# Optimization experiments

Hardware: AMD Instinct MI355X
Metric: run time of the kernel (lower is better)

## Reference

```python
import jax, jax.numpy as jnp
import numpy as np

L = 4           # num_layers
H = 1536        # hidden_size
NQ = 12         # num_q_heads
NKV = 2         # num_kv_heads
D = 128         # head_dim
I = 8960        # mlp intermediate
S = 2048        # q_len == max_seq_len (full prefill, past_kv_len = 0)
EPS = 1e-6
SCALE = 1.0 / np.sqrt(D)


def setup_inputs() -> dict:
    key = jax.random.key(0)
    ks = jax.random.split(key, 16)
    hidden_states = jax.random.normal(ks[0], (1, S, H), dtype=jnp.float32)
    # real RoPE tables (base 10000), duplicated-half layout like HF Qwen2
    inv_freq = 1.0 / (10000.0 ** (np.arange(0, D, 2, dtype=np.float32) / D))
    t = np.arange(S, dtype=np.float32)
    freqs = np.outer(t, inv_freq)                      # [S, D/2]
    emb = np.concatenate([freqs, freqs], axis=-1)      # [S, D]
    position_cos = jnp.asarray(np.cos(emb))[None]      # [1, S, D]
    position_sin = jnp.asarray(np.sin(emb))[None]
    # causal additive mask [1, 1, S, S]
    causal = jnp.tril(jnp.ones((S, S), dtype=bool))
    attention_mask = jnp.where(causal, 0.0, -1e9).astype(jnp.float32)[None, None]
    sd = 0.02
    Wq = sd * jax.random.normal(ks[1], (L, H, NQ * D), dtype=jnp.float32)
    bq = jnp.zeros((L, NQ * D), dtype=jnp.float32)
    Wk = sd * jax.random.normal(ks[2], (L, H, NKV * D), dtype=jnp.float32)
    bk = jnp.zeros((L, NKV * D), dtype=jnp.float32)
    Wv = sd * jax.random.normal(ks[3], (L, H, NKV * D), dtype=jnp.float32)
    bv = jnp.zeros((L, NKV * D), dtype=jnp.float32)
    Wo = sd * jax.random.normal(ks[4], (L, NQ * D, H), dtype=jnp.float32)
    Wgate = sd * jax.random.normal(ks[5], (L, H, I), dtype=jnp.float32)
    Wup = sd * jax.random.normal(ks[6], (L, H, I), dtype=jnp.float32)
    Wdown = sd * jax.random.normal(ks[7], (L, I, H), dtype=jnp.float32)
    ln1_w = jnp.ones((L, H), dtype=jnp.float32)
    ln2_w = jnp.ones((L, H), dtype=jnp.float32)
    final_ln_w = jnp.ones((H,), dtype=jnp.float32)
    return dict(hidden_states=hidden_states, position_cos=position_cos,
                position_sin=position_sin, attention_mask=attention_mask,
                Wq=Wq, bq=bq, Wk=Wk, bk=bk, Wv=Wv, bv=bv, Wo=Wo,
                Wgate=Wgate, Wup=Wup, Wdown=Wdown,
                ln1_w=ln1_w, ln2_w=ln2_w, final_ln_w=final_ln_w)


def rms_norm(x, w):
    return x * jax.lax.rsqrt(jnp.mean(x * x, axis=-1, keepdims=True) + EPS) * w


def rotate_half(x):
    x1, x2 = jnp.split(x, 2, axis=-1)
    return jnp.concatenate([-x2, x1], axis=-1)


def reference(hidden_states, position_cos, position_sin, attention_mask,
              Wq, bq, Wk, bk, Wv, bv, Wo, Wgate, Wup, Wdown,
              ln1_w, ln2_w, final_ln_w):
    cos = position_cos[:, None]  # [1, 1, S, D]
    sin = position_sin[:, None]
    x = hidden_states
    rep = NQ // NKV
    for i in range(L):
        residual = x
        h = rms_norm(x, ln1_w[i])
        q = (h @ Wq[i] + bq[i]).reshape(1, S, NQ, D).transpose(0, 2, 1, 3)   # [1,NQ,S,D]
        k = (h @ Wk[i] + bk[i]).reshape(1, S, NKV, D).transpose(0, 2, 1, 3)  # [1,NKV,S,D]
        v = (h @ Wv[i] + bv[i]).reshape(1, S, NKV, D).transpose(0, 2, 1, 3)
        q = q * cos + rotate_half(q) * sin
        k = k * cos + rotate_half(k) * sin
        # KV cache write is fp16; full prefill so cache == current k/v (fp16 roundtrip)
        k_full = k.astype(jnp.float16).astype(jnp.float32)
        v_full = v.astype(jnp.float16).astype(jnp.float32)
        k_full = jnp.repeat(k_full, rep, axis=1)  # GQA expand -> [1,NQ,S,D]
        v_full = jnp.repeat(v_full, rep, axis=1)
        scores = jnp.einsum('bhqd,bhkd->bhqk', q, k_full) * SCALE + attention_mask
        probs = jax.nn.softmax(scores, axis=-1)
        attn = jnp.einsum('bhqk,bhkd->bhqd', probs, v_full)
        attn = attn.transpose(0, 2, 1, 3).reshape(1, S, NQ * D)
        x = residual + attn @ Wo[i]
        residual = x
        h = rms_norm(x, ln2_w[i])
        x = residual + (jax.nn.silu(h @ Wgate[i]) * (h @ Wup[i])) @ Wdown[i]
    return rms_norm(x, final_ln_w)
```

## Files before the change

kernel.cpp:

```cpp
#include <hip/hip_runtime.h>

#define S_LEN 2048
#define H_DIM 1536
#define NQ_H 12
#define NKV_H 2
#define HD 128
#define I_DIM 8960
#define QKV_N 2048
#define GU_N 17920
#define SCALE 0.08838834764831845f

typedef _Float16 f16;
typedef _Float16 f16x8 __attribute__((ext_vector_type(8)));
typedef float f32x4 __attribute__((ext_vector_type(4)));

__device__ __forceinline__ void gload16(const void* g, void* l) {
  __builtin_amdgcn_global_load_lds((__attribute__((address_space(1))) void*)g,
                                   (__attribute__((address_space(3))) void*)l,
                                   16, 0, 0);
}

template <int MODE>
__global__ __launch_bounds__(256) void gemm_bt(const f16* __restrict__ A,
                                               const f16* __restrict__ BT,
                                               float* __restrict__ Cf,
                                               f16* __restrict__ Ch,
                                               int N, int Ktot, int Kc) {
  __shared__ __attribute__((aligned(16))) f16 As[128 * 32];
  __shared__ __attribute__((aligned(16))) f16 Bs[128 * 32];
  const int tid = threadIdx.x;
  const int w = tid >> 6, lane = tid & 63;
  const int quad = lane >> 4, cc = lane & 15;
  const int wm = w >> 1, wn = w & 1;
  const int m0 = blockIdx.y * 128, n0 = blockIdx.x * 128;
  const int kbase = blockIdx.z * Kc;

  const int c1 = tid, c2 = tid + 256;
  const f16* Ag1 = A + (size_t)(m0 + (c1 >> 2)) * Ktot + kbase + (c1 & 3) * 8;
  const f16* Ag2 = A + (size_t)(m0 + (c2 >> 2)) * Ktot + kbase + (c2 & 3) * 8;
  const f16* Bg1 = BT + (size_t)(n0 + (c1 >> 2)) * Ktot + kbase + (c1 & 3) * 8;
  const f16* Bg2 = BT + (size_t)(n0 + (c2 >> 2)) * Ktot + kbase + (c2 & 3) * 8;
  f16* Al1 = As + (w * 64) * 8;
  f16* Al2 = As + (256 + w * 64) * 8;
  f16* Bl1 = Bs + (w * 64) * 8;
  f16* Bl2 = Bs + (256 + w * 64) * 8;

  const f32x4 fz = {0.f, 0.f, 0.f, 0.f};
  f32x4 acc[4][4];
#pragma unroll
  for (int i = 0; i < 4; ++i)
#pragma unroll
    for (int j = 0; j < 4; ++j) acc[i][j] = fz;

  for (int k0 = 0; k0 < Kc; k0 += 32) {
    __syncthreads();
    gload16(Ag1 + k0, Al1);
    gload16(Ag2 + k0, Al2);
    gload16(Bg1 + k0, Bl1);
    gload16(Bg2 + k0, Bl2);
    __syncthreads();
    f16x8 af[4], bf[4];
#pragma unroll
    for (int i = 0; i < 4; ++i)
      af[i] = *(const f16x8*)(As + (wm * 64 + i * 16 + cc) * 32 + quad * 8);
#pragma unroll
    for (int j = 0; j < 4; ++j)
      bf[j] = *(const f16x8*)(Bs + (wn * 64 + j * 16 + cc) * 32 + quad * 8);
#pragma unroll
    for (int i = 0; i < 4; ++i)
#pragma unroll
      for (int j = 0; j < 4; ++j)
        acc[i][j] = __builtin_amdgcn_mfma_f32_16x16x32_f16(af[i], bf[j], acc[i][j], 0, 0, 0);
  }

#pragma unroll
  for (int i = 0; i < 4; ++i) {
    const int row = m0 + wm * 64 + i * 16 + quad * 4;
#pragma unroll
    for (int j = 0; j < 4; ++j) {
      const int col = n0 + wn * 64 + j * 16 + cc;
#pragma unroll
      for (int r = 0; r < 4; ++r) {
        const size_t idx = (size_t)(row + r) * N + col;
        if (MODE == 1) unsafeAtomicAdd(&Cf[idx], acc[i][j][r]);
        else Ch[idx] = (f16)acc[i][j][r];
      }
    }
  }
}

__global__ __launch_bounds__(256) void transpose_f2h(const float* __restrict__ src,
                                                     f16* __restrict__ dst,
                                                     int K_, int N_) {
  __shared__ float tile[32][33];
  const int c0 = blockIdx.x * 32, r0 = blockIdx.y * 32;
  const int x = threadIdx.x & 31, y4 = threadIdx.x >> 5;
#pragma unroll
  for (int i = 0; i < 4; ++i) {
    int r = r0 + y4 + i * 8;
    if (r < K_ && c0 + x < N_) tile[y4 + i * 8][x] = src[(size_t)r * N_ + c0 + x];
  }
  __syncthreads();
#pragma unroll
  for (int i = 0; i < 4; ++i) {
    int rr = y4 + i * 8;
    int dr = c0 + rr, dc = r0 + x;
    if (dr < N_ && dc < K_) dst[(size_t)dr * K_ + dc] = (f16)tile[x][rr];
  }
}

template <bool OUT_F32>
__global__ __launch_bounds__(256) void rmsnorm_kernel(const float* __restrict__ x,
                                                      const float* __restrict__ w,
                                                      f16* __restrict__ hh,
                                                      float* __restrict__ hf) {
  const int s = blockIdx.x;
  const float* xr = x + (size_t)s * H_DIM;
  float ss = 0.f;
  for (int i = threadIdx.x; i < H_DIM; i += 256) {
    float v = xr[i];
    ss += v * v;
  }
#pragma unroll
  for (int m = 32; m >= 1; m >>= 1) ss += __shfl_xor(ss, m);
  __shared__ float red[4];
  if ((threadIdx.x & 63) == 0) red[threadIdx.x >> 6] = ss;
  __syncthreads();
  ss = red[0] + red[1] + red[2] + red[3];
  const float rr = rsqrtf(ss * (1.0f / H_DIM) + 1e-6f);
  for (int i = threadIdx.x; i < H_DIM; i += 256) {
    float v = xr[i] * rr * w[i];
    if (OUT_F32) hf[(size_t)s * H_DIM + i] = v;
    else hh[(size_t)s * H_DIM + i] = (f16)v;
  }
}

__global__ __launch_bounds__(256) void rope_kernel(const float* __restrict__ qkv,
                                                   const float* __restrict__ cosb,
                                                   const float* __restrict__ sinb,
                                                   const float* __restrict__ bq,
                                                   const float* __restrict__ bk,
                                                   const float* __restrict__ bv,
                                                   f16* __restrict__ q_r,
                                                   f16* __restrict__ k_r,
                                                   f16* __restrict__ v_r) {
  const int s = blockIdx.x;
  const float* row = qkv + (size_t)s * QKV_N;
#pragma unroll
  for (int ci = 0; ci < 8; ++ci) {
    const int col = ci * 256 + threadIdx.x;
    if (col < 1536) {
      const int hh = col >> 7, d = col & 127;
      const int part = (d < 64) ? d + 64 : d - 64;
      const float v0 = row[col] + bq[col];
      const float v1 = row[(hh << 7) + part] + bq[(hh << 7) + part];
      const float cs = cosb[s * HD + d], sn = sinb[s * HD + d];
      const float rot = (d < 64) ? -v1 : v1;
      q_r[((size_t)hh * S_LEN + s) * HD + d] = (f16)(v0 * cs + rot * sn);
    } else if (col < 1792) {
      const int cc2 = col - 1536;
      const int hh = cc2 >> 7, d = cc2 & 127;
      const int part = (d < 64) ? d + 64 : d - 64;
      const float v0 = row[col] + bk[cc2];
      const float v1 = row[1536 + (hh << 7) + part] + bk[(hh << 7) + part];
      const float cs = cosb[s * HD + d], sn = sinb[s * HD + d];
      const float rot = (d < 64) ? -v1 : v1;
      k_r[((size_t)hh * S_LEN + s) * HD + d] = (f16)(v0 * cs + rot * sn);
    } else {
      const int cc2 = col - 1792;
      const int hh = cc2 >> 7, d = cc2 & 127;
      const float v0 = row[col] + bv[cc2];
      v_r[((size_t)hh * HD + d) * S_LEN + s] = (f16)v0;
    }
  }
}

__global__ __launch_bounds__(256) void attn_kernel(const f16* __restrict__ Q,
                                                   const f16* __restrict__ Kc,
                                                   const f16* __restrict__ Vt,
                                                   f16* __restrict__ Oa) {
  __shared__ __attribute__((aligned(16))) f16 ks[64 * 136];
  __shared__ __attribute__((aligned(16))) f16 vs[128 * 72];
  __shared__ __attribute__((aligned(16))) f16 ps[64 * 72];
  const int h = blockIdx.x, qt = blockIdx.y;
  const int hk = h / (NQ_H / NKV_H);
  const int tid = threadIdx.x, w = tid >> 6, lane = tid & 63;
  const int quad = lane >> 4, cc = lane & 15;

  f16x8 qf[4];
  const f16* Qg = Q + ((size_t)h * S_LEN + qt * 64) * HD;
#pragma unroll
  for (int kk = 0; kk < 4; ++kk)
    qf[kk] = *(const f16x8*)(Qg + (size_t)(w * 16 + cc) * HD + kk * 32 + quad * 8);

  const f32x4 fz = {0.f, 0.f, 0.f, 0.f};
  f32x4 o_acc[8];
  float m_run[4], l_run[4];
#pragma unroll
  for (int j = 0; j < 8; ++j) o_acc[j] = fz;
#pragma unroll
  for (int r = 0; r < 4; ++r) { m_run[r] = -1e30f; l_run[r] = 0.f; }

  const int nkt = qt + 1;
  for (int kt = 0; kt < nkt; ++kt) {
    const int kv0 = kt * 64;
    __syncthreads();
    const f16* Kg = Kc + ((size_t)hk * S_LEN + kv0) * HD;
    for (int t = tid; t < 64 * 16; t += 256) {
      int r = t >> 4, ch = t & 15;
      *(uint4*)(ks + r * 136 + ch * 8) = *(const uint4*)(Kg + (size_t)r * HD + ch * 8);
    }
    const f16* Vg = Vt + (size_t)hk * HD * S_LEN + kv0;
    for (int t = tid; t < 128 * 8; t += 256) {
      int r = t >> 3, ch = t & 7;
      *(uint4*)(vs + r * 72 + ch * 8) = *(const uint4*)(Vg + (size_t)r * S_LEN + ch * 8);
    }
    __syncthreads();

    f32x4 sc[4];
#pragma unroll
    for (int j = 0; j < 4; ++j) sc[j] = fz;
#pragma unroll
    for (int kk = 0; kk < 4; ++kk) {
      f16x8 bfr[4];
#pragma unroll
      for (int j = 0; j < 4; ++j)
        bfr[j] = *(const f16x8*)(ks + (j * 16 + cc) * 136 + kk * 32 + quad * 8);
#pragma unroll
      for (int j = 0; j < 4; ++j)
        sc[j] = __builtin_amdgcn_mfma_f32_16x16x32_f16(qf[kk], bfr[j], sc[j], 0, 0, 0);
    }

    const bool need_mask = (kt == qt);
#pragma unroll
    for (int j = 0; j < 4; ++j)
#pragma unroll
      for (int r = 0; r < 4; ++r) {
        float v = sc[j][r] * SCALE;
        if (need_mask) {
          int rowg = qt * 64 + w * 16 + quad * 4 + r;
          int colg = kv0 + j * 16 + cc;
          if (colg > rowg) v = -1e30f;
        }
        sc[j][r] = v;
      }

#pragma unroll
    for (int r = 0; r < 4; ++r) {
      float mx = sc[0][r];
#pragma unroll
      for (int j = 1; j < 4; ++j) mx = fmaxf(mx, sc[j][r]);
      mx = fmaxf(mx, __shfl_xor(mx, 1));
      mx = fmaxf(mx, __shfl_xor(mx, 2));
      mx = fmaxf(mx, __shfl_xor(mx, 4));
      mx = fmaxf(mx, __shfl_xor(mx, 8));
      const float mnew = fmaxf(m_run[r], mx);
      const float alpha = __expf(m_run[r] - mnew);
      m_run[r] = mnew;
      l_run[r] *= alpha;
#pragma unroll
      for (int jd = 0; jd < 8; ++jd) o_acc[jd][r] *= alpha;
      float rs = 0.f;
      const int prow = w * 16 + quad * 4 + r;
#pragma unroll
      for (int j = 0; j < 4; ++j) {
        float p = __expf(sc[j][r] - mnew);
        rs += p;
        ps[prow * 72 + j * 16 + cc] = (f16)p;
      }
      rs += __shfl_xor(rs, 1);
      rs += __shfl_xor(rs, 2);
      rs += __shfl_xor(rs, 4);
      rs += __shfl_xor(rs, 8);
      l_run[r] += rs;
    }

#pragma unroll
    for (int kk = 0; kk < 2; ++kk) {
      f16x8 pa = *(const f16x8*)(ps + (w * 16 + cc) * 72 + kk * 32 + quad * 8);
#pragma unroll
      for (int j = 0; j < 8; ++j) {
        f16x8 vb = *(const f16x8*)(vs + (j * 16 + cc) * 72 + kk * 32 + quad * 8);
        o_acc[j] = __builtin_amdgcn_mfma_f32_16x16x32_f16(pa, vb, o_acc[j], 0, 0, 0);
      }
    }
  }

#pragma unroll
  for (int j = 0; j < 8; ++j)
#pragma unroll
    for (int r = 0; r < 4; ++r) {
      const int rowg = qt * 64 + w * 16 + quad * 4 + r;
      const int colg = j * 16 + cc;
      Oa[(size_t)rowg * H_DIM + h * HD + colg] = (f16)(o_acc[j][r] / l_run[r]);
    }
}

__global__ __launch_bounds__(256) void silu_mul(const f16* __restrict__ gu,
                                                f16* __restrict__ hm) {
  const int i = blockIdx.x * 256 + threadIdx.x;
  const int s = blockIdx.y;
  const float g = (float)gu[(size_t)s * GU_N + i];
  const float u = (float)gu[(size_t)s * GU_N + I_DIM + i];
  const float sig = 1.f / (1.f + __expf(-g));
  hm[(size_t)s * I_DIM + i] = (f16)(g * sig * u);
}

extern "C" void kernel_launch(void* const* d_in, const int* in_sizes, int n_in,
                              void* d_out, int out_size, void* d_ws, size_t ws_size,
                              hipStream_t stream) {
  const float* hidden = (const float*)d_in[0];
  const float* cosb   = (const float*)d_in[1];
  const float* sinb   = (const float*)d_in[2];
  const float* Wq     = (const float*)d_in[4];
  const float* bq     = (const float*)d_in[5];
  const float* Wk     = (const float*)d_in[6];
  const float* bk     = (const float*)d_in[7];
  const float* Wv     = (const float*)d_in[8];
  const float* bv     = (const float*)d_in[9];
  const float* Wo     = (const float*)d_in[10];
  const float* Wg     = (const float*)d_in[11];
  const float* Wu     = (const float*)d_in[12];
  const float* Wd     = (const float*)d_in[13];
  const float* ln1    = (const float*)d_in[14];
  const float* ln2    = (const float*)d_in[15];
  const float* lnf    = (const float*)d_in[16];

  char* wp = (char*)d_ws;
  auto take = [&](size_t bytes) {
    void* p = (void*)wp;
    wp += (bytes + 255) & ~(size_t)255;
    return p;
  };
  f16* wqkvT  = (f16*)take((size_t)QKV_N * H_DIM * 2);
  f16* woT    = (f16*)take((size_t)H_DIM * H_DIM * 2);
  f16* wguT   = (f16*)take((size_t)GU_N * H_DIM * 2);
  f16* wdT    = (f16*)take((size_t)H_DIM * I_DIM * 2);
  float* x    = (float*)take((size_t)S_LEN * H_DIM * 4);
  f16* hbuf   = (f16*)take((size_t)S_LEN * H_DIM * 2);
  float* qkv  = (float*)take((size_t)S_LEN * QKV_N * 4);
  f16* q_r    = (f16*)take((size_t)NQ_H * S_LEN * HD * 2);
  f16* k_r    = (f16*)take((size_t)NKV_H * S_LEN * HD * 2);
  f16* v_r    = (f16*)take((size_t)NKV_H * HD * S_LEN * 2);
  f16* gu     = (f16*)take((size_t)S_LEN * GU_N * 2);
  f16* hmid   = (f16*)take((size_t)S_LEN * I_DIM * 2);

  hipMemcpyAsync(x, hidden, (size_t)S_LEN * H_DIM * 4, hipMemcpyDeviceToDevice, stream);

  for (int l = 0; l < 4; ++l) {
    transpose_f2h<<<dim3(48, 48), 256, 0, stream>>>(Wq + (size_t)l * H_DIM * 1536, wqkvT, H_DIM, 1536);
    transpose_f2h<<<dim3(8, 48), 256, 0, stream>>>(Wk + (size_t)l * H_DIM * 256, wqkvT + (size_t)1536 * H_DIM, H_DIM, 256);
    transpose_f2h<<<dim3(8, 48), 256, 0, stream>>>(Wv + (size_t)l * H_DIM * 256, wqkvT + (size_t)1792 * H_DIM, H_DIM, 256);
    transpose_f2h<<<dim3(48, 48), 256, 0, stream>>>(Wo + (size_t)l * H_DIM * H_DIM, woT, H_DIM, H_DIM);
    transpose_f2h<<<dim3(280, 48), 256, 0, stream>>>(Wg + (size_t)l * H_DIM * I_DIM, wguT, H_DIM, I_DIM);
    transpose_f2h<<<dim3(280, 48), 256, 0, stream>>>(Wu + (size_t)l * H_DIM * I_DIM, wguT + (size_t)I_DIM * H_DIM, H_DIM, I_DIM);
    transpose_f2h<<<dim3(48, 280), 256, 0, stream>>>(Wd + (size_t)l * I_DIM * H_DIM, wdT, I_DIM, H_DIM);

    rmsnorm_kernel<false><<<S_LEN, 256, 0, stream>>>(x, ln1 + l * H_DIM, hbuf, nullptr);
    hipMemsetAsync(qkv, 0, (size_t)S_LEN * QKV_N * 4, stream);
    gemm_bt<1><<<dim3(QKV_N / 128, S_LEN / 128, 2), 256, 0, stream>>>(hbuf, wqkvT, qkv, nullptr, QKV_N, H_DIM, 768);
    rope_kernel<<<S_LEN, 256, 0, stream>>>(qkv, cosb, sinb, bq + l * 1536, bk + l * 256, bv + l * 256, q_r, k_r, v_r);
    attn_kernel<<<dim3(NQ_H, S_LEN / 64), 256, 0, stream>>>(q_r, k_r, v_r, hbuf);
    gemm_bt<1><<<dim3(H_DIM / 128, S_LEN / 128, 4), 256, 0, stream>>>(hbuf, woT, x, nullptr, H_DIM, H_DIM, 384);
    rmsnorm_kernel<false><<<S_LEN, 256, 0, stream>>>(x, ln2 + l * H_DIM, hbuf, nullptr);
    gemm_bt<2><<<dim3(GU_N / 128, S_LEN / 128, 1), 256, 0, stream>>>(hbuf, wguT, nullptr, gu, GU_N, H_DIM, H_DIM);
    silu_mul<<<dim3(I_DIM / 256, S_LEN), 256, 0, stream>>>(gu, hmid);
    gemm_bt<1><<<dim3(H_DIM / 128, S_LEN / 128, 4), 256, 0, stream>>>(hmid, wdT, x, nullptr, H_DIM, I_DIM, 2240);
  }
  rmsnorm_kernel<true><<<S_LEN, 256, 0, stream>>>(x, lnf, nullptr, (float*)d_out);
}
```

Before: 3.098 ms.

## Add 256x256-tile 8-wave GEMM with 4-stage LDS pipeline for QKV, gate/up, down

Adds a new GEMM kernel that uses 256x256 output tiles with 512 threads, each wave computing a 128x64 subtile. It keeps a four-buffer LDS ring with async global-to-LDS loads issued three steps ahead, interleaved with the MFMA work, and uses XOR-swizzled LDS addressing. The QKV, gate/up and down projections now use it, with new split-K factors. This raises operand reuse and overlaps loads with math, at the cost of high register pressure and fewer blocks for the smaller GEMMs.

```diff
diff --git a/kernel.cpp b/kernel.cpp
--- a/kernel.cpp
+++ b/kernel.cpp
@@ -18,6 +18,129 @@
   __builtin_amdgcn_global_load_lds((__attribute__((address_space(1))) void*)g,
                                    (__attribute__((address_space(3))) void*)l,
                                    16, 0, 0);
+}
+
+template <int MODE>
+__global__ __launch_bounds__(512, 2) void gemm256(const f16* __restrict__ A,
+                                                  const f16* __restrict__ BT,
+                                                  float* __restrict__ Cf,
+                                                  f16* __restrict__ Ch,
+                                                  int N, int Ktot, int Kc) {
+  constexpr int TE = 256 * 32;
+  __shared__ __attribute__((aligned(16))) f16 As[4 * TE];
+  __shared__ __attribute__((aligned(16))) f16 Bs[4 * TE];
+  const int tid = threadIdx.x;
+  const int w = tid >> 6, lane = tid & 63;
+  const int quad = lane >> 4, cc = lane & 15;
+  const int wm = w >> 2, wn = w & 3;
+  const int m0 = blockIdx.y * 256, n0 = blockIdx.x * 256;
+  const int kbase = blockIdx.z * Kc;
+  const int NT = Kc >> 5;
+
+  const int lr = lane >> 2, lc = lane & 3;
+  const int cg = lc ^ (lr & 3) ^ ((lr >> 2) & 1);
+  const f16* AgR0 = A + (size_t)(m0 + w * 16 + lr) * Ktot + kbase + cg * 8;
+  const f16* AgR1 = AgR0 + (size_t)128 * Ktot;
+  const f16* BgR0 = BT + (size_t)(n0 + w * 16 + lr) * Ktot + kbase + cg * 8;
+  const f16* BgR1 = BgR0 + (size_t)128 * Ktot;
+  const int ldsl0 = (w * 16) * 32;
+  const int ldsl1 = (128 + w * 16) * 32;
+
+  const int sc8 = (quad ^ (cc & 3) ^ ((cc >> 2) & 1)) * 8;
+
+  const f32x4 fz = {0.f, 0.f, 0.f, 0.f};
+  f32x4 acc[8][4];
+#pragma unroll
+  for (int i = 0; i < 8; ++i)
+#pragma unroll
+    for (int j = 0; j < 4; ++j) acc[i][j] = fz;
+
+#pragma unroll
+  for (int pt = 0; pt < 3; ++pt) {
+    const int kk = pt * 32;
+    gload16(AgR0 + kk, As + pt * TE + ldsl0);
+    gload16(AgR1 + kk, As + pt * TE + ldsl1);
+    gload16(BgR0 + kk, Bs + pt * TE + ldsl0);
+    gload16(BgR1 + kk, Bs + pt * TE + ldsl1);
+  }
+
+  for (int t = 0; t < NT; ++t) {
+    const f16* Ab = As + (t & 3) * TE;
+    const f16* Bb = Bs + (t & 3) * TE;
+    const int ahead = NT - 1 - t;
+    if (ahead >= 2)      asm volatile("s_waitcnt vmcnt(8)" ::: "memory");
+    else if (ahead == 1) asm volatile("s_waitcnt vmcnt(4)" ::: "memory");
+    else                 asm volatile("s_waitcnt vmcnt(0)" ::: "memory");
+    asm volatile("s_barrier" ::: "memory");
+
+    const bool pf = (t + 3) < NT;
+    const int kq = (t + 3) * 32;
+    f16* Apf = As + ((t + 3) & 3) * TE;
+    f16* Bpf = Bs + ((t + 3) & 3) * TE;
+
+    f16x8 bf[4], af0, af1;
+
+    if (pf) gload16(AgR0 + kq, Apf + ldsl0);
+#pragma unroll
+    for (int fc = 0; fc < 4; ++fc)
+      bf[fc] = *(const f16x8*)(Bb + (wn * 64 + fc * 16 + cc) * 32 + sc8);
+    af0 = *(const f16x8*)(Ab + (wm * 128 + 0 * 16 + cc) * 32 + sc8);
+    af1 = *(const f16x8*)(Ab + (wm * 128 + 1 * 16 + cc) * 32 + sc8);
+#pragma unroll
+    for (int fc = 0; fc < 4; ++fc)
+      acc[0][fc] = __builtin_amdgcn_mfma_f32_16x16x32_f16(af0, bf[fc], acc[0][fc], 0, 0, 0);
+#pragma unroll
+    for (int fc = 0; fc < 4; ++fc)
+      acc[1][fc] = __builtin_amdgcn_mfma_f32_16x16x32_f16(af1, bf[fc], acc[1][fc], 0, 0, 0);
+    asm volatile("s_barrier" ::: "memory");
+
+    if (pf) gload16(AgR1 + kq, Apf + ldsl1);
+    af0 = *(const f16x8*)(Ab + (wm * 128 + 2 * 16 + cc) * 32 + sc8);
+    af1 = *(const f16x8*)(Ab + (wm * 128 + 3 * 16 + cc) * 32 + sc8);
+#pragma unroll
+    for (int fc = 0; fc < 4; ++fc)
+      acc[2][fc] = __builtin_amdgcn_mfma_f32_16x16x32_f16(af0, bf[fc], acc[2][fc], 0, 0, 0);
+#pragma unroll
+    for (int fc = 0; fc < 4; ++fc)
+      acc[3][fc] = __builtin_amdgcn_mfma_f32_16x16x32_f16(af1, bf[fc], acc[3][fc], 0, 0, 0);
+    asm volatile("s_barrier" ::: "memory");
+
+    if (pf) gload16(BgR0 + kq, Bpf + ldsl0);
+    af0 = *(const f16x8*)(Ab + (wm * 128 + 4 * 16 + cc) * 32 + sc8);
+    af1 = *(const f16x8*)(Ab + (wm * 128 + 5 * 16 + cc) * 32 + sc8);
+#pragma unroll
+    for (int fc = 0; fc < 4; ++fc)
+      acc[4][fc] = __builtin_amdgcn_mfma_f32_16x16x32_f16(af0, bf[fc], acc[4][fc], 0, 0, 0);
+#pragma unroll
+    for (int fc = 0; fc < 4; ++fc)
+      acc[5][fc] = __builtin_amdgcn_mfma_f32_16x16x32_f16(af1, bf[fc], acc[5][fc], 0, 0, 0);
+    asm volatile("s_barrier" ::: "memory");
+
+    if (pf) gload16(BgR1 + kq, Bpf + ldsl1);
+    af0 = *(const f16x8*)(Ab + (wm * 128 + 6 * 16 + cc) * 32 + sc8);
+    af1 = *(const f16x8*)(Ab + (wm * 128 + 7 * 16 + cc) * 32 + sc8);
+#pragma unroll
+    for (int fc = 0; fc < 4; ++fc)
+      acc[6][fc] = __builtin_amdgcn_mfma_f32_16x16x32_f16(af0, bf[fc], acc[6][fc], 0, 0, 0);
+#pragma unroll
+    for (int fc = 0; fc < 4; ++fc)
+      acc[7][fc] = __builtin_amdgcn_mfma_f32_16x16x32_f16(af1, bf[fc], acc[7][fc], 0, 0, 0);
+  }
+
+#pragma unroll
+  for (int fr = 0; fr < 8; ++fr) {
+    const int row = m0 + wm * 128 + fr * 16 + quad * 4;
+#pragma unroll
+    for (int fc = 0; fc < 4; ++fc) {
+      const int col = n0 + wn * 64 + fc * 16 + cc;
+#pragma unroll
+      for (int r = 0; r < 4; ++r) {
+        const size_t idx = (size_t)(row + r) * N + col;
+        if (MODE == 1) unsafeAtomicAdd(&Cf[idx], acc[fr][fc][r]);
+        else Ch[idx] = (f16)acc[fr][fc][r];
+      }
+    }
+  }
 }
 
 template <int MODE>
@@ -358,14 +481,14 @@
 
     rmsnorm_kernel<false><<<S_LEN, 256, 0, stream>>>(x, ln1 + l * H_DIM, hbuf, nullptr);
     hipMemsetAsync(qkv, 0, (size_t)S_LEN * QKV_N * 4, stream);
-    gemm_bt<1><<<dim3(QKV_N / 128, S_LEN / 128, 2), 256, 0, stream>>>(hbuf, wqkvT, qkv, nullptr, QKV_N, H_DIM, 768);
+    gemm256<1><<<dim3(QKV_N / 256, S_LEN / 256, 4), 512, 0, stream>>>(hbuf, wqkvT, qkv, nullptr, QKV_N, H_DIM, 384);
     rope_kernel<<<S_LEN, 256, 0, stream>>>(qkv, cosb, sinb, bq + l * 1536, bk + l * 256, bv + l * 256, q_r, k_r, v_r);
     attn_kernel<<<dim3(NQ_H, S_LEN / 64), 256, 0, stream>>>(q_r, k_r, v_r, hbuf);
     gemm_bt<1><<<dim3(H_DIM / 128, S_LEN / 128, 4), 256, 0, stream>>>(hbuf, woT, x, nullptr, H_DIM, H_DIM, 384);
     rmsnorm_kernel<false><<<S_LEN, 256, 0, stream>>>(x, ln2 + l * H_DIM, hbuf, nullptr);
-    gemm_bt<2><<<dim3(GU_N / 128, S_LEN / 128, 1), 256, 0, stream>>>(hbuf, wguT, nullptr, gu, GU_N, H_DIM, H_DIM);
+    gemm256<2><<<dim3(GU_N / 256, S_LEN / 256, 1), 512, 0, stream>>>(hbuf, wguT, nullptr, gu, GU_N, H_DIM, H_DIM);
     silu_mul<<<dim3(I_DIM / 256, S_LEN), 256, 0, stream>>>(gu, hmid);
-    gemm_bt<1><<<dim3(H_DIM / 128, S_LEN / 128, 4), 256, 0, stream>>>(hmid, wdT, x, nullptr, H_DIM, I_DIM, 2240);
+    gemm256<1><<<dim3(H_DIM / 256, S_LEN / 256, 5), 512, 0, stream>>>(hmid, wdT, x, nullptr, H_DIM, I_DIM, 1792);
   }
   rmsnorm_kernel<true><<<S_LEN, 256, 0, stream>>>(x, lnf, nullptr, (float*)d_out);
 }
```

After: 3.630 ms. 1.17x slower.

## Add 256x256-tile 4-stage pipelined GEMM for QKV, gate/up and down projections

Applied to the files above, without the earlier changes.

Introduces a 512-thread GEMM kernel with 256x256 output tiles, a 4-slot LDS ring filled by direct global-to-LDS loads three tiles ahead, XOR-swizzled LDS addressing, and raised wave priority around the MFMA block. It is used for the QKV, gate/up and down projections, with split-K factors changed to keep the grid filled. The aim is more operand reuse per LDS load and better hiding of load latency than the 128x128 kernel. In exchange it uses 128 KB of LDS and 128 accumulator registers per thread, which limits occupancy, and the larger tiles give fewer blocks (the gate/up grid is 70x8).

```diff
diff --git a/kernel.cpp b/kernel.cpp
--- a/kernel.cpp
+++ b/kernel.cpp
@@ -18,6 +18,100 @@
   __builtin_amdgcn_global_load_lds((__attribute__((address_space(1))) void*)g,
                                    (__attribute__((address_space(3))) void*)l,
                                    16, 0, 0);
+}
+
+template <int MODE>
+__global__ __launch_bounds__(512, 2) void gemm256(const f16* __restrict__ A,
+                                                  const f16* __restrict__ BT,
+                                                  float* __restrict__ Cf,
+                                                  f16* __restrict__ Ch,
+                                                  int N, int Ktot, int Kc) {
+  constexpr int TS = 256 * 32;
+  __shared__ __attribute__((aligned(16))) f16 As[4 * TS];
+  __shared__ __attribute__((aligned(16))) f16 Bs[4 * TS];
+  const int tid = threadIdx.x;
+  const int w = tid >> 6, lane = tid & 63;
+  const int quad = lane >> 4, cc = lane & 15;
+  const int wm = w >> 2, wn = w & 3;
+  const int m0 = blockIdx.y * 256, n0 = blockIdx.x * 256;
+  const int kbase = blockIdx.z * Kc;
+  const int NT = Kc >> 5;
+
+  const int srow = lane >> 2;
+  const int schk = lane & 3;
+  const int gchk = schk ^ (srow & 3);
+  const f16* Ag = A + (size_t)(m0 + w * 32 + srow) * Ktot + kbase + gchk * 8;
+  const f16* Bg = BT + (size_t)(n0 + w * 32 + srow) * Ktot + kbase + gchk * 8;
+  const int lb = (w * 32) * 32;
+
+  const int rs8 = (quad ^ (cc & 3)) * 8;
+
+  const f32x4 fz = {0.f, 0.f, 0.f, 0.f};
+  f32x4 acc[8][4];
+#pragma unroll
+  for (int i = 0; i < 8; ++i)
+#pragma unroll
+    for (int j = 0; j < 4; ++j) acc[i][j] = fz;
+
+#define STAGE256(slot, tt)                                   \
+  {                                                          \
+    f16* Ad = As + (slot)*TS + lb;                           \
+    f16* Bd = Bs + (slot)*TS + lb;                           \
+    const int ko = (tt)*32;                                  \
+    gload16(Ag + ko, Ad);                                    \
+    gload16(Ag + ko + 16 * Ktot, Ad + 16 * 32);              \
+    gload16(Bg + ko, Bd);                                    \
+    gload16(Bg + ko + 16 * Ktot, Bd + 16 * 32);              \
+  }
+
+  STAGE256(0, 0);
+  STAGE256(1, 1);
+  STAGE256(2, 2);
+
+  for (int t = 0; t < NT; ++t) {
+    const int ahead = NT - 1 - t;
+    if (ahead >= 2)      asm volatile("s_waitcnt vmcnt(8)" ::: "memory");
+    else if (ahead == 1) asm volatile("s_waitcnt vmcnt(4)" ::: "memory");
+    else                 asm volatile("s_waitcnt vmcnt(0)" ::: "memory");
+    asm volatile("s_barrier" ::: "memory");
+
+    const f16* Ab = As + (t & 3) * TS;
+    const f16* Bb = Bs + (t & 3) * TS;
+
+    f16x8 bf[4], af[8];
+#pragma unroll
+    for (int nf = 0; nf < 4; ++nf)
+      bf[nf] = *(const f16x8*)(Bb + (wn * 64 + nf * 16 + cc) * 32 + rs8);
+#pragma unroll
+    for (int mf = 0; mf < 8; ++mf)
+      af[mf] = *(const f16x8*)(Ab + (wm * 128 + mf * 16 + cc) * 32 + rs8);
+
+    __builtin_amdgcn_s_setprio(1);
+#pragma unroll
+    for (int mf = 0; mf < 8; ++mf)
+#pragma unroll
+      for (int nf = 0; nf < 4; ++nf)
+        acc[mf][nf] = __builtin_amdgcn_mfma_f32_16x16x32_f16(af[mf], bf[nf], acc[mf][nf], 0, 0, 0);
+    __builtin_amdgcn_s_setprio(0);
+
+    if (t + 3 < NT) STAGE256((t + 3) & 3, t + 3);
+  }
+#undef STAGE256
+
+#pragma unroll
+  for (int fr = 0; fr < 8; ++fr) {
+    const int row = m0 + wm * 128 + fr * 16 + quad * 4;
+#pragma unroll
+    for (int fc = 0; fc < 4; ++fc) {
+      const int col = n0 + wn * 64 + fc * 16 + cc;
+#pragma unroll
+      for (int r = 0; r < 4; ++r) {
+        const size_t idx = (size_t)(row + r) * N + col;
+        if (MODE == 1) unsafeAtomicAdd(&Cf[idx], acc[fr][fc][r]);
+        else Ch[idx] = (f16)acc[fr][fc][r];
+      }
+    }
+  }
 }
 
 template <int MODE>
@@ -358,14 +452,14 @@
 
     rmsnorm_kernel<false><<<S_LEN, 256, 0, stream>>>(x, ln1 + l * H_DIM, hbuf, nullptr);
     hipMemsetAsync(qkv, 0, (size_t)S_LEN * QKV_N * 4, stream);
-    gemm_bt<1><<<dim3(QKV_N / 128, S_LEN / 128, 2), 256, 0, stream>>>(hbuf, wqkvT, qkv, nullptr, QKV_N, H_DIM, 768);
+    gemm256<1><<<dim3(QKV_N / 256, S_LEN / 256, 4), 512, 0, stream>>>(hbuf, wqkvT, qkv, nullptr, QKV_N, H_DIM, 384);
     rope_kernel<<<S_LEN, 256, 0, stream>>>(qkv, cosb, sinb, bq + l * 1536, bk + l * 256, bv + l * 256, q_r, k_r, v_r);
     attn_kernel<<<dim3(NQ_H, S_LEN / 64), 256, 0, stream>>>(q_r, k_r, v_r, hbuf);
     gemm_bt<1><<<dim3(H_DIM / 128, S_LEN / 128, 4), 256, 0, stream>>>(hbuf, woT, x, nullptr, H_DIM, H_DIM, 384);
     rmsnorm_kernel<false><<<S_LEN, 256, 0, stream>>>(x, ln2 + l * H_DIM, hbuf, nullptr);
-    gemm_bt<2><<<dim3(GU_N / 128, S_LEN / 128, 1), 256, 0, stream>>>(hbuf, wguT, nullptr, gu, GU_N, H_DIM, H_DIM);
+    gemm256<2><<<dim3(GU_N / 256, S_LEN / 256, 1), 512, 0, stream>>>(hbuf, wguT, nullptr, gu, GU_N, H_DIM, H_DIM);
     silu_mul<<<dim3(I_DIM / 256, S_LEN), 256, 0, stream>>>(gu, hmid);
-    gemm_bt<1><<<dim3(H_DIM / 128, S_LEN / 128, 4), 256, 0, stream>>>(hmid, wdT, x, nullptr, H_DIM, I_DIM, 2240);
+    gemm256<1><<<dim3(H_DIM / 256, S_LEN / 256, 5), 512, 0, stream>>>(hmid, wdT, x, nullptr, H_DIM, I_DIM, 1792);
   }
   rmsnorm_kernel<true><<<S_LEN, 256, 0, stream>>>(x, lnf, nullptr, (float*)d_out);
 }
```

After: 3.086 ms. About the same (-0.4%).
